# Kernel tuning notes

Measured on AMD Instinct MI355X. Metric: run time of the kernel, lower is better.

The kernel has to match this reference:

```python
import jax, jax.numpy as jnp
import numpy as np


def _cell(x, h, c, Wih, Whh, bih, bhh):
    # torch.nn.LSTMCell gate order: i, f, g, o
    gates = x @ Wih.T + h @ Whh.T + bih + bhh  # [B, 4H]
    i, f, g, o = jnp.split(gates, 4, axis=-1)
    i = jax.nn.sigmoid(i)
    f = jax.nn.sigmoid(f)
    g = jnp.tanh(g)
    o = jax.nn.sigmoid(o)
    c_new = f * c + i * g
    h_new = o * jnp.tanh(c_new)
    return h_new, c_new


def setup_inputs() -> dict:
    key = jax.random.key(0)
    B, T, D, H = 4096, 256, 4, 16
    ks = jax.random.split(key, 32)
    s = 1.0 / np.sqrt(H)  # torch LSTMCell/Linear uniform init bound

    def u(k, shape):
        return jax.random.uniform(k, shape, jnp.float32, -s, s)

    inp = {"y": jax.random.normal(ks[0], (B, T, D), jnp.float32)}
    names = ["f1", "f2", "f3", "b1", "b2", "b3"]
    ins = [D, H, H, D, H, H]
    idx = 1
    for n, di in zip(names, ins):
        inp[f"Wih_{n}"] = u(ks[idx], (4 * H, di)); idx += 1
        inp[f"Whh_{n}"] = u(ks[idx], (4 * H, H)); idx += 1
        inp[f"bih_{n}"] = u(ks[idx], (4 * H,)); idx += 1
        inp[f"bhh_{n}"] = u(ks[idx], (4 * H,)); idx += 1
    inp["W_out"] = u(ks[idx], (4, 2 * H)); idx += 1
    inp["b_out"] = u(ks[idx], (4,))
    return inp


def reference(y,
              Wih_f1, Whh_f1, bih_f1, bhh_f1,
              Wih_f2, Whh_f2, bih_f2, bhh_f2,
              Wih_f3, Whh_f3, bih_f3, bhh_f3,
              Wih_b1, Whh_b1, bih_b1, bhh_b1,
              Wih_b2, Whh_b2, bih_b2, bhh_b2,
              Wih_b3, Whh_b3, bih_b3, bhh_b3,
              W_out, b_out):
    B = y.shape[0]
    H = Whh_f1.shape[1]
    z = jnp.zeros((B, H), y.dtype)
    carry0 = (z, z, z, z, z, z, z, z, z, z, z, z)
    # forward-time and reversed-time sequences, time-major for scan: [T, B, 4]
    xs = (jnp.swapaxes(y, 0, 1), jnp.swapaxes(y[:, ::-1, :], 0, 1))

    def step(carry, x_t):
        hf1, cf1, hf2, cf2, hf3, cf3, hb1, cb1, hb2, cb2, hb3, cb3 = carry
        xf, xb = x_t
        hf1, cf1 = _cell(xf, hf1, cf1, Wih_f1, Whh_f1, bih_f1, bhh_f1)
        hf2, cf2 = _cell(hf1, hf2, cf2, Wih_f2, Whh_f2, bih_f2, bhh_f2)
        hf3, cf3 = _cell(hf2, hf3, cf3, Wih_f3, Whh_f3, bih_f3, bhh_f3)
        hb1, cb1 = _cell(xb, hb1, cb1, Wih_b1, Whh_b1, bih_b1, bhh_b1)
        hb2, cb2 = _cell(hb1, hb2, cb2, Wih_b2, Whh_b2, bih_b2, bhh_b2)
        hb3, cb3 = _cell(hb2, hb3, cb3, Wih_b3, Whh_b3, bih_b3, bhh_b3)
        return (hf1, cf1, hf2, cf2, hf3, cf3, hb1, cb1, hb2, cb2, hb3, cb3), None

    carry, _ = jax.lax.scan(step, carry0, xs)
    hf3, hb3 = carry[4], carry[10]
    out = jnp.concatenate([hf3, hb3], axis=1) @ W_out.T + b_out  # [B, 4]
    return out[:, None, :]  # [B, 1, 4]
```

## Files before the change

kernel.cpp:

```cpp
#include <hip/hip_runtime.h>

#define T_LEN 256
#define D_IN 4
#define NSTEP (T_LEN + 2)

typedef __fp16 h8 __attribute__((ext_vector_type(8)));
typedef __fp16 cvt2_t __attribute__((ext_vector_type(2)));
typedef float float4v __attribute__((ext_vector_type(4)));

struct CellW { const float *Wih, *Whh, *bih, *bhh; };
struct Params { CellW c[6]; const float* y; float* hout; };

__device__ __forceinline__ float fexp2(float x) { return __builtin_amdgcn_exp2f(x); }
__device__ __forceinline__ float frcp(float x)  { return __builtin_amdgcn_rcpf(x); }
__device__ __forceinline__ int packh(float a, float b) {
    cvt2_t p = __builtin_amdgcn_cvt_pkrtz(a, b);
    return __builtin_bit_cast(int, p);
}
__device__ __forceinline__ h8 mk8(int a, int b, int c, int d) {
    int4 v; v.x = a; v.y = b; v.z = c; v.w = d;
    return __builtin_bit_cast(h8, v);
}

#define MFMA32(a, b, c) __builtin_amdgcn_mfma_f32_16x16x32_f16(a, b, c, 0, 0, 0)

__device__ __forceinline__ void act2(const float4v& pA, const float4v& pB,
                                     float& cA, float& cB,
                                     float& hA, float& hB) {
    float eiA = fexp2(pA[0]), efA = fexp2(pA[1]), egA = fexp2(pA[2]);
    float eiB = fexp2(pB[0]), efB = fexp2(pB[1]), egB = fexp2(pB[2]);
    float FA = 1.f + efA,              FB = 1.f + efB;
    float PA = (1.f + eiA) * (1.f + egA), PB = (1.f + eiB) * (1.f + egB);
    float NGA = 1.f - egA,             NGB = 1.f - egB;
    float denA = FA * PA,              denB = FB * PB;
    float numA = fmaf(cA, PA, NGA * FA);
    float numB = fmaf(cB, PB, NGB * FB);
    float RC = frcp(denA * denB);
    cA = numA * denB * RC;
    cB = numB * denA * RC;
    const float K2 = -2.8853900817779268f;
    float eoA = fexp2(pA[3]), ecA = fexp2(fminf(cA * K2, 30.f));
    float eoB = fexp2(pB[3]), ecB = fexp2(fminf(cB * K2, 30.f));
    float NOA = 1.f - ecA,    NOB = 1.f - ecB;
    float DhA = (1.f + eoA) * (1.f + ecA);
    float DhB = (1.f + eoB) * (1.f + ecB);
    float RH = frcp(DhA * DhB);
    hA = NOA * DhB * RH;
    hB = NOB * DhA * RH;
}

__global__ void __launch_bounds__(384)
__attribute__((amdgpu_waves_per_eu(3, 4)))
lstm_wf_kernel(Params p)
{
    __shared__ int2 x_lds[T_LEN][16];
    __shared__ int h_pk[2][3][2][4][16];

    const int tid = threadIdx.x;
    const int v = tid >> 6;
    const int l = v >> 1;
    const int e = v & 1;
    const int L = tid & 63;
    const int n = L & 15;
    const int Q = L >> 4;

    const int dir = blockIdx.x & 1;
    const int b0  = (blockIdx.x >> 1) * 16;
    const CellW cw = p.c[dir * 3 + l];
    const float LOG2E = 1.4426950408889634f;

    for (int i = tid; i < 2 * 3 * 2 * 4 * 16; i += 384)
        ((int*)h_pk)[i] = 0;
    for (int i = tid; i < T_LEN * 16; i += 384) {
        const int t = i >> 4, nn = i & 15;
        const int tt = dir ? (T_LEN - 1 - t) : t;
        const float4 xv = *(const float4*)(p.y +
            ((size_t)(b0 + nn) * T_LEN + tt) * D_IN);
        int2 xp; xp.x = packh(xv.x, xv.y); xp.y = packh(xv.z, xv.w);
        x_lds[t][nn] = xp;
    }

    const int gate = n & 3;
    const int su = n >> 2;
    const float sA = (gate == 2) ? -2.f * LOG2E : -LOG2E;
    h8 A8[2];
    float4v bs[2];
#pragma unroll
    for (int j = 0; j < 2; ++j) {
        const int u = 8 * e + 4 * j + su;
        const int row = gate * 16 + u;
        float vh[4], vp[4];
#pragma unroll
        for (int i = 0; i < 4; ++i) {
            const int col = 4 * i + Q;
            vh[i] = cw.Whh[row * 16 + col];
            vp[i] = (l == 0) ? ((Q == 0) ? cw.Wih[row * D_IN + i] : 0.f)
                             : cw.Wih[row * 16 + col];
        }
        A8[j] = mk8(packh(vh[0] * sA, vh[1] * sA), packh(vh[2] * sA, vh[3] * sA),
                    packh(vp[0] * sA, vp[1] * sA), packh(vp[2] * sA, vp[3] * sA));
        const int ub = 8 * e + 4 * j + Q;
        const float br0 = cw.bih[0 * 16 + ub] + cw.bhh[0 * 16 + ub];
        const float br1 = cw.bih[1 * 16 + ub] + cw.bhh[1 * 16 + ub];
        const float br2 = cw.bih[2 * 16 + ub] + cw.bhh[2 * 16 + ub];
        const float br3 = cw.bih[3 * 16 + ub] + cw.bhh[3 * 16 + ub];
        bs[j] = (float4v){br0 * -LOG2E, br1 * -LOG2E,
                          br2 * -2.f * LOG2E, br3 * -LOG2E};
    }

    __syncthreads();

    float cA = 0.f, cB = 0.f;
    float hA = 0.f, hB = 0.f;

#pragma unroll 1
    for (int s = 0; s < NSTEP; ++s) {
        if (s >= l && s - l < T_LEN) {
            const int t = s - l;
            const int pr = (s + 1) & 1;
            const int* hsO = &h_pk[pr][l][0][Q][n];
            const int o0 = hsO[0];
            const int o1 = hsO[64];
            int pd0, pd1;
            if (l == 0) {
                const int2 xv = x_lds[t][n];
                pd0 = (Q == 0) ? xv.x : 0;
                pd1 = (Q == 0) ? xv.y : 0;
            } else {
                const int* hsP = &h_pk[pr][l - 1][0][Q][n];
                pd0 = hsP[0];
                pd1 = hsP[64];
            }
            const h8 b8 = mk8(o0, o1, pd0, pd1);
            float4v p0 = MFMA32(A8[0], b8, bs[0]);
            float4v p1 = MFMA32(A8[1], b8, bs[1]);
            act2(p0, p1, cA, cB, hA, hB);
            const int pw = s & 1;
            h_pk[pw][l][e][Q][n] = packh(hA, hB);
        }
        __syncthreads();
    }

    if (l == 2) {
        float* o = p.hout + (size_t)(b0 + n) * 32 + dir * 16;
        o[8 * e + Q]     = hA;
        o[8 * e + 4 + Q] = hB;
    }
}

__global__ void out_proj_kernel(const float* __restrict__ ws,
                                const float* __restrict__ Wout,
                                const float* __restrict__ bout,
                                float* __restrict__ out, int B)
{
    int idx = blockIdx.x * blockDim.x + threadIdx.x;
    if (idx >= B * 4) return;
    int b = idx >> 2, o = idx & 3;
    float acc = bout[o];
    const float* h = ws + (size_t)b * 32;
    const float* w = Wout + o * 32;
#pragma unroll
    for (int m = 0; m < 32; ++m) acc = fmaf(h[m], w[m], acc);
    out[idx] = acc;
}

extern "C" void kernel_launch(void* const* d_in, const int* in_sizes, int n_in,
                              void* d_out, int out_size, void* d_ws, size_t ws_size,
                              hipStream_t stream)
{
    const int B = in_sizes[0] / (T_LEN * D_IN);

    Params p;
    for (int s = 0; s < 6; ++s) {
        p.c[s].Wih = (const float*)d_in[1 + 4 * s];
        p.c[s].Whh = (const float*)d_in[2 + 4 * s];
        p.c[s].bih = (const float*)d_in[3 + 4 * s];
        p.c[s].bhh = (const float*)d_in[4 + 4 * s];
    }
    p.y = (const float*)d_in[0];
    p.hout = (float*)d_ws;

    const int blocks = (B / 16) * 2;
    lstm_wf_kernel<<<blocks, 384, 0, stream>>>(p);

    const float* Wout = (const float*)d_in[25];
    const float* bout = (const float*)d_in[26];
    out_proj_kernel<<<(B * 4 + 255) / 256, 256, 0, stream>>>(
        (const float*)d_ws, Wout, bout, (float*)d_out, B);
}
```

Baseline: 257.4 us.

## Merge forward and backward directions into one 768-thread block with LDS padding

Each block now runs both LSTM directions for 16 batch rows using 12 waves, where before separate blocks handled each direction. The per-direction x and h buffers are duplicated in shared memory. A dummy LDS array, kept alive by a single store, pads LDS use, apparently to cap how many blocks share a CU. Every step's barrier now syncs 12 waves instead of 6, so one slow direction can stall the other, in exchange for fewer blocks and a different occupancy pattern.

```diff
diff --git a/kernel.cpp b/kernel.cpp
--- a/kernel.cpp
+++ b/kernel.cpp
@@ -49,35 +49,41 @@
     hB = NOB * DhA * RH;
 }
 
-__global__ void __launch_bounds__(384)
+__global__ void __launch_bounds__(768)
 __attribute__((amdgpu_waves_per_eu(3, 4)))
 lstm_wf_kernel(Params p)
 {
-    __shared__ int2 x_lds[T_LEN][16];
-    __shared__ int h_pk[2][3][2][4][16];
+    __shared__ int2 x_lds[2][T_LEN][16];
+    __shared__ int h_pk[2][2][3][2][4][16];
+    __shared__ int pad_excl[3072];
 
     const int tid = threadIdx.x;
     const int v = tid >> 6;
-    const int l = v >> 1;
-    const int e = v & 1;
+    const int half = (v >= 6);
+    const int v6 = v - 6 * half;
+    const int l = v6 >> 1;
+    const int e = v6 & 1;
     const int L = tid & 63;
     const int n = L & 15;
     const int Q = L >> 4;
 
-    const int dir = blockIdx.x & 1;
-    const int b0  = (blockIdx.x >> 1) * 16;
-    const CellW cw = p.c[dir * 3 + l];
+    const int b0 = blockIdx.x * 16;
+    const CellW cw = p.c[half * 3 + l];
     const float LOG2E = 1.4426950408889634f;
 
-    for (int i = tid; i < 2 * 3 * 2 * 4 * 16; i += 384)
+    if (tid == 767) pad_excl[0] = tid;
+
+    for (int i = tid; i < 2 * 2 * 3 * 2 * 4 * 16; i += 768)
         ((int*)h_pk)[i] = 0;
-    for (int i = tid; i < T_LEN * 16; i += 384) {
-        const int t = i >> 4, nn = i & 15;
-        const int tt = dir ? (T_LEN - 1 - t) : t;
+    for (int i = tid; i < 2 * T_LEN * 16; i += 768) {
+        const int d = i >> 12;
+        const int r = i & 4095;
+        const int t = r >> 4, nn = r & 15;
+        const int tt = d ? (T_LEN - 1 - t) : t;
         const float4 xv = *(const float4*)(p.y +
             ((size_t)(b0 + nn) * T_LEN + tt) * D_IN);
         int2 xp; xp.x = packh(xv.x, xv.y); xp.y = packh(xv.z, xv.w);
-        x_lds[t][nn] = xp;
+        x_lds[d][t][nn] = xp;
     }
 
     const int gate = n & 3;
@@ -118,16 +124,16 @@
         if (s >= l && s - l < T_LEN) {
             const int t = s - l;
             const int pr = (s + 1) & 1;
-            const int* hsO = &h_pk[pr][l][0][Q][n];
+            const int* hsO = &h_pk[half][pr][l][0][Q][n];
             const int o0 = hsO[0];
             const int o1 = hsO[64];
             int pd0, pd1;
             if (l == 0) {
-                const int2 xv = x_lds[t][n];
+                const int2 xv = x_lds[half][t][n];
                 pd0 = (Q == 0) ? xv.x : 0;
                 pd1 = (Q == 0) ? xv.y : 0;
             } else {
-                const int* hsP = &h_pk[pr][l - 1][0][Q][n];
+                const int* hsP = &h_pk[half][pr][l - 1][0][Q][n];
                 pd0 = hsP[0];
                 pd1 = hsP[64];
             }
@@ -136,13 +142,13 @@
             float4v p1 = MFMA32(A8[1], b8, bs[1]);
             act2(p0, p1, cA, cB, hA, hB);
             const int pw = s & 1;
-            h_pk[pw][l][e][Q][n] = packh(hA, hB);
+            h_pk[half][pw][l][e][Q][n] = packh(hA, hB);
         }
         __syncthreads();
     }
 
     if (l == 2) {
-        float* o = p.hout + (size_t)(b0 + n) * 32 + dir * 16;
+        float* o = p.hout + (size_t)(b0 + n) * 32 + half * 16;
         o[8 * e + Q]     = hA;
         o[8 * e + 4 + Q] = hB;
     }
@@ -180,8 +186,8 @@
     p.y = (const float*)d_in[0];
     p.hout = (float*)d_ws;
 
-    const int blocks = (B / 16) * 2;
-    lstm_wf_kernel<<<blocks, 384, 0, stream>>>(p);
+    const int blocks = B / 16;
+    lstm_wf_kernel<<<blocks, 768, 0, stream>>>(p);
 
     const float* Wout = (const float*)d_in[25];
     const float* bout = (const float*)d_in[26];
```

Result: faster. 243.2 us (-5.5%).

## Run all three layers per wave and pack both directions into one block

Applied to the files above, without the earlier changes.

Each wave now computes all three stacked LSTM layers of one direction, skewed by one timestep, so the three independent MFMA and activation chains interleave within a single wave. One block of 256 threads covers both directions for 16 batch rows, giving one block per CU. A 96 KB dynamic shared-memory pad is requested to enforce that occupancy. Input x is prefetched from global memory in chunks of 8 steps into registers, replacing the earlier LDS staging of the whole sequence. The trade-off is more work per wave on each step and fewer resident waves to hide latency, with a block barrier still taken every step.

```diff
diff --git a/kernel.cpp b/kernel.cpp
--- a/kernel.cpp
+++ b/kernel.cpp
@@ -2,7 +2,8 @@
 
 #define T_LEN 256
 #define D_IN 4
-#define NSTEP (T_LEN + 2)
+#define SPR 8
+#define NROUND 33
 
 typedef __fp16 h8 __attribute__((ext_vector_type(8)));
 typedef __fp16 cvt2_t __attribute__((ext_vector_type(2)));
@@ -49,103 +50,146 @@
     hB = NOB * DhA * RH;
 }
 
-__global__ void __launch_bounds__(384)
-__attribute__((amdgpu_waves_per_eu(3, 4)))
+__global__ void __launch_bounds__(256)
 lstm_wf_kernel(Params p)
 {
-    __shared__ int2 x_lds[T_LEN][16];
-    __shared__ int h_pk[2][3][2][4][16];
+    extern __shared__ int dyn_pad[];
+    __shared__ int h_sl[2][2][2][3][4][16];
 
     const int tid = threadIdx.x;
     const int v = tid >> 6;
-    const int l = v >> 1;
+    const int dir = v >> 1;
     const int e = v & 1;
     const int L = tid & 63;
     const int n = L & 15;
     const int Q = L >> 4;
 
-    const int dir = blockIdx.x & 1;
-    const int b0  = (blockIdx.x >> 1) * 16;
-    const CellW cw = p.c[dir * 3 + l];
+    const int b0 = blockIdx.x * 16;
     const float LOG2E = 1.4426950408889634f;
 
-    for (int i = tid; i < 2 * 3 * 2 * 4 * 16; i += 384)
-        ((int*)h_pk)[i] = 0;
-    for (int i = tid; i < T_LEN * 16; i += 384) {
-        const int t = i >> 4, nn = i & 15;
-        const int tt = dir ? (T_LEN - 1 - t) : t;
-        const float4 xv = *(const float4*)(p.y +
-            ((size_t)(b0 + nn) * T_LEN + tt) * D_IN);
-        int2 xp; xp.x = packh(xv.x, xv.y); xp.y = packh(xv.z, xv.w);
-        x_lds[t][nn] = xp;
-    }
+    if (p.y == nullptr) dyn_pad[0] = 1;
+
+    for (int i = tid; i < 2 * 2 * 2 * 3 * 4 * 16; i += 256)
+        ((int*)h_sl)[i] = 0;
 
     const int gate = n & 3;
     const int su = n >> 2;
     const float sA = (gate == 2) ? -2.f * LOG2E : -LOG2E;
-    h8 A8[2];
-    float4v bs[2];
-#pragma unroll
-    for (int j = 0; j < 2; ++j) {
-        const int u = 8 * e + 4 * j + su;
-        const int row = gate * 16 + u;
-        float vh[4], vp[4];
-#pragma unroll
-        for (int i = 0; i < 4; ++i) {
-            const int col = 4 * i + Q;
-            vh[i] = cw.Whh[row * 16 + col];
-            vp[i] = (l == 0) ? ((Q == 0) ? cw.Wih[row * D_IN + i] : 0.f)
-                             : cw.Wih[row * 16 + col];
-        }
-        A8[j] = mk8(packh(vh[0] * sA, vh[1] * sA), packh(vh[2] * sA, vh[3] * sA),
-                    packh(vp[0] * sA, vp[1] * sA), packh(vp[2] * sA, vp[3] * sA));
-        const int ub = 8 * e + 4 * j + Q;
-        const float br0 = cw.bih[0 * 16 + ub] + cw.bhh[0 * 16 + ub];
-        const float br1 = cw.bih[1 * 16 + ub] + cw.bhh[1 * 16 + ub];
-        const float br2 = cw.bih[2 * 16 + ub] + cw.bhh[2 * 16 + ub];
-        const float br3 = cw.bih[3 * 16 + ub] + cw.bhh[3 * 16 + ub];
-        bs[j] = (float4v){br0 * -LOG2E, br1 * -LOG2E,
-                          br2 * -2.f * LOG2E, br3 * -LOG2E};
+    h8 A8[3][2];
+    float4v bs[3][2];
+#pragma unroll
+    for (int l = 0; l < 3; ++l) {
+        const CellW cw = p.c[dir * 3 + l];
+#pragma unroll
+        for (int j = 0; j < 2; ++j) {
+            const int u = 8 * e + 4 * j + su;
+            const int row = gate * 16 + u;
+            float vh[4], vp[4];
+#pragma unroll
+            for (int i = 0; i < 4; ++i) {
+                const int col = 4 * i + Q;
+                vh[i] = cw.Whh[row * 16 + col];
+                vp[i] = (l == 0) ? ((Q == 0) ? cw.Wih[row * D_IN + i] : 0.f)
+                                 : cw.Wih[row * 16 + col];
+            }
+            A8[l][j] = mk8(packh(vh[0]*sA, vh[1]*sA), packh(vh[2]*sA, vh[3]*sA),
+                           packh(vp[0]*sA, vp[1]*sA), packh(vp[2]*sA, vp[3]*sA));
+            const int ub = 8 * e + 4 * j + Q;
+            const float br0 = cw.bih[0 * 16 + ub] + cw.bhh[0 * 16 + ub];
+            const float br1 = cw.bih[1 * 16 + ub] + cw.bhh[1 * 16 + ub];
+            const float br2 = cw.bih[2 * 16 + ub] + cw.bhh[2 * 16 + ub];
+            const float br3 = cw.bih[3 * 16 + ub] + cw.bhh[3 * 16 + ub];
+            bs[l][j] = (float4v){br0 * -LOG2E, br1 * -LOG2E,
+                                 br2 * -2.f * LOG2E, br3 * -LOG2E};
+        }
+    }
+
+    const float* ybase = p.y + (size_t)(b0 + n) * (T_LEN * D_IN);
+    int2 xq[SPR], xn[SPR];
+    if (L < 16) {
+#pragma unroll
+        for (int k = 0; k < SPR; ++k) {
+            const int tt = dir ? (T_LEN - 1 - k) : k;
+            const float4 xv = *(const float4*)(ybase + (size_t)tt * D_IN);
+            xq[k].x = packh(xv.x, xv.y);
+            xq[k].y = packh(xv.z, xv.w);
+        }
     }
 
     __syncthreads();
 
-    float cA = 0.f, cB = 0.f;
-    float hA = 0.f, hB = 0.f;
+    float c0[3] = {0.f, 0.f, 0.f};
+    float c1[3] = {0.f, 0.f, 0.f};
+    float h0[3] = {0.f, 0.f, 0.f};
+    float h1[3] = {0.f, 0.f, 0.f};
+    int own[3] = {0, 0, 0};
 
 #pragma unroll 1
-    for (int s = 0; s < NSTEP; ++s) {
-        if (s >= l && s - l < T_LEN) {
-            const int t = s - l;
+    for (int r = 0; r < NROUND; ++r) {
+        if (L < 16) {
+#pragma unroll
+            for (int k = 0; k < SPR; ++k) {
+                const int t = SPR * (r + 1) + k;
+                if (t < T_LEN) {
+                    const int tt = dir ? (T_LEN - 1 - t) : t;
+                    const float4 xv = *(const float4*)(ybase + (size_t)tt * D_IN);
+                    xn[k].x = packh(xv.x, xv.y);
+                    xn[k].y = packh(xv.z, xv.w);
+                }
+            }
+        }
+
+#pragma unroll
+        for (int k = 0; k < SPR; ++k) {
+            const int s = SPR * r + k;
             const int pr = (s + 1) & 1;
-            const int* hsO = &h_pk[pr][l][0][Q][n];
-            const int o0 = hsO[0];
-            const int o1 = hsO[64];
-            int pd0, pd1;
-            if (l == 0) {
-                const int2 xv = x_lds[t][n];
-                pd0 = (Q == 0) ? xv.x : 0;
-                pd1 = (Q == 0) ? xv.y : 0;
-            } else {
-                const int* hsP = &h_pk[pr][l - 1][0][Q][n];
-                pd0 = hsP[0];
-                pd1 = hsP[64];
-            }
-            const h8 b8 = mk8(o0, o1, pd0, pd1);
-            float4v p0 = MFMA32(A8[0], b8, bs[0]);
-            float4v p1 = MFMA32(A8[1], b8, bs[1]);
-            act2(p0, p1, cA, cB, hA, hB);
             const int pw = s & 1;
-            h_pk[pw][l][e][Q][n] = packh(hA, hB);
-        }
-        __syncthreads();
-    }
-
-    if (l == 2) {
-        float* o = p.hout + (size_t)(b0 + n) * 32 + dir * 16;
-        o[8 * e + Q]     = hA;
-        o[8 * e + 4 + Q] = hB;
-    }
+            const int sib0 = h_sl[pr][dir][1 - e][0][Q][n];
+            const int sib1 = h_sl[pr][dir][1 - e][1][Q][n];
+            const int sib2 = h_sl[pr][dir][1 - e][2][Q][n];
+
+            const int x0 = (Q == 0) ? xq[k].x : 0;
+            const int x1 = (Q == 0) ? xq[k].y : 0;
+            const h8 b80 = mk8(e ? sib0 : own[0], e ? own[0] : sib0, x0, x1);
+            const h8 b81 = mk8(e ? sib1 : own[1], e ? own[1] : sib1,
+                               e ? sib0 : own[0], e ? own[0] : sib0);
+            const h8 b82 = mk8(e ? sib2 : own[2], e ? own[2] : sib2,
+                               e ? sib1 : own[1], e ? own[1] : sib1);
+
+            const bool a0 = (s < T_LEN);
+            const bool a1 = (s >= 1) && (s - 1 < T_LEN);
+            const bool a2 = (s >= 2) && (s - 2 < T_LEN);
+
+            float4v p00, p01, p10, p11, p20, p21;
+            if (a0) { p00 = MFMA32(A8[0][0], b80, bs[0][0]);
+                      p01 = MFMA32(A8[0][1], b80, bs[0][1]); }
+            if (a1) { p10 = MFMA32(A8[1][0], b81, bs[1][0]);
+                      p11 = MFMA32(A8[1][1], b81, bs[1][1]); }
+            if (a2) { p20 = MFMA32(A8[2][0], b82, bs[2][0]);
+                      p21 = MFMA32(A8[2][1], b82, bs[2][1]); }
+
+            if (a0) { act2(p00, p01, c0[0], c1[0], h0[0], h1[0]);
+                      own[0] = packh(h0[0], h1[0]); }
+            if (a1) { act2(p10, p11, c0[1], c1[1], h0[1], h1[1]);
+                      own[1] = packh(h0[1], h1[1]); }
+            if (a2) { act2(p20, p21, c0[2], c1[2], h0[2], h1[2]);
+                      own[2] = packh(h0[2], h1[2]); }
+
+            h_sl[pw][dir][e][0][Q][n] = own[0];
+            h_sl[pw][dir][e][1][Q][n] = own[1];
+            h_sl[pw][dir][e][2][Q][n] = own[2];
+            __syncthreads();
+        }
+
+        if (L < 16) {
+#pragma unroll
+            for (int k = 0; k < SPR; ++k) xq[k] = xn[k];
+        }
+    }
+
+    float* o = p.hout + (size_t)(b0 + n) * 32 + dir * 16;
+    o[8 * e + Q]     = h0[2];
+    o[8 * e + 4 + Q] = h1[2];
 }
 
 __global__ void out_proj_kernel(const float* __restrict__ ws,
@@ -180,8 +224,8 @@
     p.y = (const float*)d_in[0];
     p.hout = (float*)d_ws;
 
-    const int blocks = (B / 16) * 2;
-    lstm_wf_kernel<<<blocks, 384, 0, stream>>>(p);
+    const int blocks = B / 16;
+    lstm_wf_kernel<<<blocks, 256, 96 * 1024, stream>>>(p);
 
     const float* Wout = (const float*)d_in[25];
     const float* bout = (const float*)d_in[26];
```

Result: slower. 313.3 us (+21.7%).
